# Kernel tuning notes

Measured on AMD Instinct MI355X. Metric: run time of the kernel, lower is better.

The kernel has to match this reference:

```python
import jax, jax.numpy as jnp
import numpy as np

B, H, W, C = 2, 256, 256, 180
WS, OWS, NH = 8, 12, 6  # window, overlap window, heads
RPB_N = (WS + OWS - 1) ** 2  # 361


def _ln(x, w, b):
    mu = x.mean(-1, keepdims=True)
    var = ((x - mu) ** 2).mean(-1, keepdims=True)
    return (x - mu) / jnp.sqrt(var + 1e-5) * w + b


def _dwt2(x):  # (b,h,w,c) -> (b,h/2,w/2,4c) haar, order [LL,LH,HL,HH]
    a = x[:, 0::2, 0::2]
    bb = x[:, 0::2, 1::2]
    cc = x[:, 1::2, 0::2]
    dd = x[:, 1::2, 1::2]
    ll = (a + bb + cc + dd) * 0.5
    lh = (-a - bb + cc + dd) * 0.5
    hl = (-a + bb - cc + dd) * 0.5
    hh = (a - bb - cc + dd) * 0.5
    return jnp.concatenate([ll, lh, hl, hh], axis=-1)


def _idwt2(y):  # (b,h2,w2,4c) -> (b,2h2,2w2,c)
    ll, lh, hl, hh = jnp.split(y, 4, axis=-1)
    a = (ll - lh - hl + hh) * 0.5
    bb = (ll - lh + hl - hh) * 0.5
    cc = (ll + lh - hl - hh) * 0.5
    dd = (ll + lh + hl + hh) * 0.5
    b_, h2, w2, c = a.shape
    even = jnp.stack([a, bb], axis=3).reshape(b_, h2, 2 * w2, c)
    odd = jnp.stack([cc, dd], axis=3).reshape(b_, h2, 2 * w2, c)
    return jnp.stack([even, odd], axis=2).reshape(b_, 2 * h2, 2 * w2, c)


def _win_part(x, ws):  # (b,h,w,c) -> (b*nw, ws, ws, c)
    b, h, w, c = x.shape
    x = x.reshape(b, h // ws, ws, w // ws, ws, c)
    return x.transpose(0, 1, 3, 2, 4, 5).reshape(-1, ws, ws, c)


def _win_rev(win, ws, h, w):  # inverse of _win_part
    b = win.shape[0] // ((h // ws) * (w // ws))
    x = win.reshape(b, h // ws, w // ws, ws, ws, -1)
    return x.transpose(0, 1, 3, 2, 4, 5).reshape(b, h, w, -1)


def _unfold_windows(x, ws, ows):  # nn.Unfold(kernel=ows, stride=ws, pad=ows-ws)
    b, hs, wss, c = x.shape
    pad = ows - ws
    xp = jnp.pad(x, ((0, 0), (pad, pad), (pad, pad), (0, 0)))
    nwh = hs // ws
    idx = (jnp.arange(nwh) * ws)[:, None] + jnp.arange(ows)[None, :]  # (nwh, ows)
    p = xp[:, idx][:, :, :, idx]  # (b, nwh, ows, nwh, ows, c)
    p = p.transpose(0, 1, 3, 2, 4, 5)  # (b, ih, iw, kh, kw, c)
    return p.reshape(b * nwh * nwh, ows * ows, c)


def _forward(x, cross_x, rpi, h, w, norm1_w, norm1_b, normc_w, normc_b,
             q_w, q_b, k_w, k_b, v_w, v_b, rpb, proj_w, proj_b,
             norm2_w, norm2_b, fc1_w, fc1_b, fc2_w, fc2_b):
    b, _, c = x.shape
    shortcut = x
    xn = _ln(x, norm1_w, norm1_b).reshape(b, h, w, c)
    _ = _ln(cross_x, normc_w, normc_b)  # computed in original wav branch, unused
    xd = _dwt2(xn)  # (b, h/2, w/2, 4c)
    q = xd @ q_w + q_b  # (b, h/2, w/2, c)
    k = xd @ k_w + k_b  # (b, h/2, w/2, c)
    v = xd @ v_w + v_b  # (b, h/2, w/2, 4c)
    scale = (c // NH) ** -0.5
    qw = _win_part(q, WS).reshape(-1, WS * WS, c)
    kw = _unfold_windows(k, WS, OWS)
    vw = _unfold_windows(v, WS, OWS)
    b_, nq = qw.shape[0], WS * WS
    n, d = OWS * OWS, c // NH
    qh = qw.reshape(b_, nq, NH, d).transpose(0, 2, 1, 3) * scale
    kh = kw.reshape(b_, n, NH, d).transpose(0, 2, 1, 3)
    vh = vw.reshape(b_, n, NH, 4 * d).transpose(0, 2, 1, 3)
    bias = rpb[rpi.reshape(-1)].reshape(nq, n, NH).transpose(2, 0, 1)  # (NH,nq,n)
    attn = jax.nn.softmax(jnp.einsum('bhqd,bhkd->bhqk', qh, kh) + bias[None], axis=-1)
    o = jnp.einsum('bhqk,bhkd->bhqd', attn, vh).transpose(0, 2, 1, 3).reshape(b_, nq, 4 * c)
    o = o.reshape(-1, WS, WS, 4 * c)
    xw = _win_rev(o, WS, h // 2, w // 2)  # (b, h/2, w/2, 4c)
    xr = _idwt2(xw).reshape(b, h * w, c)
    x1 = xr @ proj_w + proj_b + shortcut
    y = _ln(x1, norm2_w, norm2_b)
    y = jax.nn.gelu(y @ fc1_w + fc1_b, approximate=False) @ fc2_w + fc2_b
    return x1 + y


def setup_inputs() -> dict:
    key = jax.random.key(0)
    ks = jax.random.split(key, 12)
    nrm = lambda k, s: (jax.random.normal(k, s, jnp.float32) * 0.02)
    return {
        'x': jax.random.normal(ks[0], (B, H * W, C), jnp.float32),
        'cross_x': jax.random.normal(ks[1], (B, H * W, C), jnp.float32),
        'rpi': jax.random.randint(ks[2], (WS * WS, OWS * OWS), 0, RPB_N),
        'h': H, 'w': W,
        'norm1_w': jnp.ones((C,), jnp.float32), 'norm1_b': jnp.zeros((C,), jnp.float32),
        'normc_w': jnp.ones((C,), jnp.float32), 'normc_b': jnp.zeros((C,), jnp.float32),
        'q_w': nrm(ks[3], (4 * C, C)), 'q_b': jnp.zeros((C,), jnp.float32),
        'k_w': nrm(ks[4], (4 * C, C)), 'k_b': jnp.zeros((C,), jnp.float32),
        'v_w': nrm(ks[5], (4 * C, 4 * C)), 'v_b': jnp.zeros((4 * C,), jnp.float32),
        'rpb': nrm(ks[6], (RPB_N, NH)),
        'proj_w': nrm(ks[7], (C, C)), 'proj_b': jnp.zeros((C,), jnp.float32),
        'norm2_w': jnp.ones((C,), jnp.float32), 'norm2_b': jnp.zeros((C,), jnp.float32),
        'fc1_w': nrm(ks[8], (C, 2 * C)), 'fc1_b': jnp.zeros((2 * C,), jnp.float32),
        'fc2_w': nrm(ks[9], (2 * C, C)), 'fc2_b': jnp.zeros((C,), jnp.float32),
    }


def reference(x, cross_x, rpi, h, w, norm1_w, norm1_b, normc_w, normc_b,
              q_w, q_b, k_w, k_b, v_w, v_b, rpb, proj_w, proj_b,
              norm2_w, norm2_b, fc1_w, fc1_b, fc2_w, fc2_b):
    return _forward(x, cross_x, rpi, h, w, norm1_w, norm1_b, normc_w, normc_b,
                    q_w, q_b, k_w, k_b, v_w, v_b, rpb, proj_w, proj_b,
                    norm2_w, norm2_b, fc1_w, fc1_b, fc2_w, fc2_b)
```

## Files before the change

kernel.cpp:

```cpp
#include <hip/hip_runtime.h>
#include <hip/hip_bf16.h>
#include <stdint.h>

using bf16 = __hip_bfloat16;
typedef __attribute__((ext_vector_type(8))) short bf16x8;
typedef __attribute__((ext_vector_type(4))) float f32x4;

union U8 { uint4 u; bf16x8 h; };

static __device__ __forceinline__ float b2f(bf16 v) { return __bfloat162float(v); }
static __device__ __forceinline__ bf16  f2b(float v) { return __float2bfloat16(v); }
static __device__ __forceinline__ float toF(float v) { return v; }
static __device__ __forceinline__ float toF(bf16 v)  { return __bfloat162float(v); }
static __device__ __forceinline__ void stF(float* p, float v) { *p = v; }
static __device__ __forceinline__ void stF(bf16* p,  float v) { *p = f2b(v); }
static __device__ __forceinline__ float bfu(unsigned short x) {
  union { unsigned int i; float f; } z; z.i = ((unsigned int)x) << 16; return z.f;
}

__global__ __launch_bounds__(256) void convert_wt_kernel(
    const float* __restrict__ w, bf16* __restrict__ wt, int K, int N, int Kp)
{
  int idx = blockIdx.x * 256 + threadIdx.x;
  if (idx >= N * Kp) return;
  int n = idx / Kp, k = idx % Kp;
  float v = (k < K) ? w[(size_t)k * N + n] : 0.f;
  wt[idx] = f2b(v);
}

__global__ __launch_bounds__(256) void bias_pre_kernel(
    const int* __restrict__ rpi, const float* __restrict__ rpb, float* __restrict__ bias_f)
{
  int e = blockIdx.x * 256 + threadIdx.x;
  if (e >= 6 * 64 * 144) return;
  int hh = e / 9216, rk = e % 9216;
  bias_f[e] = rpb[rpi[rk] * 6 + hh];
}

__global__ __launch_bounds__(256) void ln_dwt_kernel(
    const float* __restrict__ x, const float* __restrict__ w, const float* __restrict__ bia,
    bf16* __restrict__ xd)
{
  __shared__ float nrm[4][180];
  int blk = blockIdx.x;
  int j = blk & 127; int i = (blk >> 7) & 127; int b = blk >> 14;
  int wave = threadIdx.x >> 6, lane = threadIdx.x & 63;
  int ty = wave >> 1, tx = wave & 1;
  size_t tok = (size_t)b * 65536 + (size_t)(2 * i + ty) * 256 + (size_t)(2 * j + tx);
  const float* xp = x + tok * 180;
  float v0 = xp[lane];
  float v1 = xp[lane + 64];
  float v2 = (lane < 52) ? xp[lane + 128] : 0.f;
  float s = v0 + v1 + v2, ss = v0 * v0 + v1 * v1 + v2 * v2;
  #pragma unroll
  for (int m = 32; m; m >>= 1) { s += __shfl_xor(s, m); ss += __shfl_xor(ss, m); }
  float mu = s * (1.f / 180.f);
  float rstd = rsqrtf(ss * (1.f / 180.f) - mu * mu + 1e-5f);
  nrm[wave][lane]      = (v0 - mu) * rstd * w[lane]      + bia[lane];
  nrm[wave][lane + 64] = (v1 - mu) * rstd * w[lane + 64] + bia[lane + 64];
  if (lane < 52)
    nrm[wave][lane + 128] = (v2 - mu) * rstd * w[lane + 128] + bia[lane + 128];
  __syncthreads();
  bf16* op = xd + (size_t)blk * 720;
  for (int o = threadIdx.x; o < 720; o += 256) {
    int g = o / 180, c = o % 180;
    float a = nrm[0][c], bb = nrm[1][c], cc = nrm[2][c], dd = nrm[3][c];
    float r = (g == 0) ? (a + bb + cc + dd)
            : (g == 1) ? (-a - bb + cc + dd)
            : (g == 2) ? (-a + bb - cc + dd)
                       : (a - bb - cc + dd);
    op[o] = f2b(r * 0.5f);
  }
}

__global__ __launch_bounds__(256) void ln_kernel(
    const bf16* __restrict__ x, const float* __restrict__ w, const float* __restrict__ bia,
    bf16* __restrict__ y)
{
  int wave = threadIdx.x >> 6, lane = threadIdx.x & 63;
  size_t tok = (size_t)blockIdx.x * 4 + wave;
  const bf16* xp = x + tok * 180;
  float v0 = b2f(xp[lane]);
  float v1 = b2f(xp[lane + 64]);
  float v2 = (lane < 52) ? b2f(xp[lane + 128]) : 0.f;
  float s = v0 + v1 + v2, ss = v0 * v0 + v1 * v1 + v2 * v2;
  #pragma unroll
  for (int m = 32; m; m >>= 1) { s += __shfl_xor(s, m); ss += __shfl_xor(ss, m); }
  float mu = s * (1.f / 180.f);
  float rstd = rsqrtf(ss * (1.f / 180.f) - mu * mu + 1e-5f);
  bf16* yp = y + tok * 192;
  yp[lane]      = f2b((v0 - mu) * rstd * w[lane]      + bia[lane]);
  yp[lane + 64] = f2b((v1 - mu) * rstd * w[lane + 64] + bia[lane + 64]);
  if (lane < 52)
    yp[lane + 128] = f2b((v2 - mu) * rstd * w[lane + 128] + bia[lane + 128]);
  else
    yp[lane + 128] = f2b(0.f);
}

template <int EP, typename TRes, typename TOut>
__global__ __launch_bounds__(256) void gemm_mfma(
    const bf16* __restrict__ A, const bf16* __restrict__ Wt,
    const float* __restrict__ bias, const TRes* __restrict__ res,
    TOut* __restrict__ out, int N, int KlimA, int lda, int Kp, int ldout, int ldres)
{
  __shared__ __align__(16) short Al[128 * 32];
  __shared__ __align__(16) short Bl[64 * 32];
  int tid = threadIdx.x;
  int wave = tid >> 6, lane = tid & 63;
  int wy = wave >> 1, wx = wave & 1;
  int m0 = blockIdx.x * 128, n0 = blockIdx.y * 64;

  f32x4 acc[4][2] = {};

  int ar = tid >> 2;
  int ac = (tid & 3) * 8;
  int brow = n0 + ar;
  int browc = (brow < N) ? brow : (N - 1);
  bool bvalid = (brow < N);
  const uint4* ga0 = (const uint4*)(A + (size_t)(m0 + ar) * lda + ac);
  const uint4* ga1 = (const uint4*)(A + (size_t)(m0 + 64 + ar) * lda + ac);
  const uint4* gb  = (const uint4*)(Wt + (size_t)browc * Kp + ac);

  int fm = lane & 15, quad = lane >> 4;
  const short* afp = &Al[(wy * 64 + fm) * 32 + quad * 8];
  const short* bfp = &Bl[(wx * 32 + fm) * 32 + quad * 8];

  for (int k0 = 0; k0 < Kp; k0 += 32) {
    bool avalid = (k0 + ac) < KlimA;
    uint4 za = avalid ? ga0[k0 / 8] : make_uint4(0, 0, 0, 0);
    uint4 zb = avalid ? ga1[k0 / 8] : make_uint4(0, 0, 0, 0);
    uint4 zc = bvalid ? gb[k0 / 8]  : make_uint4(0, 0, 0, 0);
    __syncthreads();
    *(uint4*)&Al[tid * 8]        = za;
    *(uint4*)&Al[2048 + tid * 8] = zb;
    *(uint4*)&Bl[tid * 8]        = zc;
    __syncthreads();

    bf16x8 af0 = *(const bf16x8*)(afp);
    bf16x8 af1 = *(const bf16x8*)(afp + 16 * 32);
    bf16x8 af2 = *(const bf16x8*)(afp + 32 * 32);
    bf16x8 af3 = *(const bf16x8*)(afp + 48 * 32);
    bf16x8 bf0 = *(const bf16x8*)(bfp);
    bf16x8 bf1 = *(const bf16x8*)(bfp + 16 * 32);

    acc[0][0] = __builtin_amdgcn_mfma_f32_16x16x32_bf16(af0, bf0, acc[0][0], 0, 0, 0);
    acc[0][1] = __builtin_amdgcn_mfma_f32_16x16x32_bf16(af0, bf1, acc[0][1], 0, 0, 0);
    acc[1][0] = __builtin_amdgcn_mfma_f32_16x16x32_bf16(af1, bf0, acc[1][0], 0, 0, 0);
    acc[1][1] = __builtin_amdgcn_mfma_f32_16x16x32_bf16(af1, bf1, acc[1][1], 0, 0, 0);
    acc[2][0] = __builtin_amdgcn_mfma_f32_16x16x32_bf16(af2, bf0, acc[2][0], 0, 0, 0);
    acc[2][1] = __builtin_amdgcn_mfma_f32_16x16x32_bf16(af2, bf1, acc[2][1], 0, 0, 0);
    acc[3][0] = __builtin_amdgcn_mfma_f32_16x16x32_bf16(af3, bf0, acc[3][0], 0, 0, 0);
    acc[3][1] = __builtin_amdgcn_mfma_f32_16x16x32_bf16(af3, bf1, acc[3][1], 0, 0, 0);
  }

  #pragma unroll
  for (int nt = 0; nt < 2; nt++) {
    int col = n0 + wx * 32 + nt * 16 + fm;
    if (col >= N) continue;
    float bv = bias[col];
    #pragma unroll
    for (int mt = 0; mt < 4; mt++) {
      int row0 = m0 + wy * 64 + mt * 16 + quad * 4;
      #pragma unroll
      for (int r = 0; r < 4; r++) {
        int row = row0 + r;
        float v = acc[mt][nt][r] + bv;
        if constexpr (EP == 1) v += toF(res[(size_t)row * ldres + col]);
        if constexpr (EP == 2) v = 0.5f * v * (1.f + erff(v * 0.70710678118654752f));
        stF(&out[(size_t)row * ldout + col], v);
      }
    }
  }
}

__global__ __launch_bounds__(256) void attn_kernel(
    const bf16* __restrict__ q, const bf16* __restrict__ k, const bf16* __restrict__ v,
    const float* __restrict__ bias_f, bf16* __restrict__ xw)
{
  __shared__ short tokl[160];
  __shared__ __align__(16) short Pl[64 * 168];
  __shared__ __align__(16) short Vt[128 * 168];
  const float scale = 0.18257418583505536f;
  int blk = blockIdx.x;
  int hh = blk % 6; int wid = blk / 6;
  int wj = wid & 15; int wi = (wid >> 4) & 15; int b = wid >> 8;
  int tid = threadIdx.x;
  int wave = tid >> 6, lane = tid & 63;
  int fm = lane & 15, quad = lane >> 4;
  const unsigned int* qu = (const unsigned int*)q;
  const unsigned int* ku = (const unsigned int*)k;
  const unsigned int* vu = (const unsigned int*)v;
  int hh15 = hh * 15, hh60 = hh * 60;

  if (tid < 144) {
    int ky = tid / 12, kx = tid % 12;
    int gy = wi * 8 - 4 + ky, gx = wj * 8 - 4 + kx;
    tokl[tid] = (gy >= 0 && gy < 128 && gx >= 0 && gx < 128)
              ? (short)(b * 16384 + gy * 128 + gx) : (short)-1;
  }
  __syncthreads();

  {
    int kg = tid & 15, oct = tid >> 4;
    int colx = (oct & 1) << 4;
    #pragma unroll
    for (int p = 0; p < 10; p++) {
      int kk = p * 16 + kg;
      int t = (kk < 144) ? (int)tokl[kk] : -1;
      U8 vv; vv.u = make_uint4(0, 0, 0, 0);
      if (oct < 15 && t >= 0)
        vv.u = *(const uint4*)(vu + (size_t)t * 360 + hh60 + oct * 4);
      short* wp = &Vt[oct * 8 * 168 + (kk ^ colx)];
      #pragma unroll
      for (int jj = 0; jj < 8; jj++) wp[jj * 168] = vv.h[jj];
    }
  }

  f32x4 sacc[9] = {};
  {
    U8 qf;
    int r = wave * 16 + fm;
    int gy = wi * 8 + (r >> 3), gx = wj * 8 + (r & 7);
    const unsigned int* qp = qu + (size_t)(b * 16384 + gy * 128 + gx) * 90 + hh15 + quad * 4;
    qf.u.x = qp[0]; qf.u.y = qp[1]; qf.u.z = qp[2]; qf.u.w = qp[3];
    if (quad == 3) qf.u.w = 0;
    #pragma unroll
    for (int nt = 0; nt < 9; nt++) {
      int t = (int)tokl[nt * 16 + fm];
      U8 kf; kf.u = make_uint4(0, 0, 0, 0);
      if (t >= 0) {
        const unsigned int* kp = ku + (size_t)t * 90 + hh15 + quad * 4;
        kf.u.x = kp[0]; kf.u.y = kp[1]; kf.u.z = kp[2]; kf.u.w = kp[3];
      }
      if (quad == 3) kf.u.w = 0;
      sacc[nt] = __builtin_amdgcn_mfma_f32_16x16x32_bf16(qf.h, kf.h, sacc[nt], 0, 0, 0);
    }
  }

  float sv[9][4];
  const float* bias_g = bias_f + hh * 9216;
  {
    #pragma unroll
    for (int r = 0; r < 4; r++) {
      int row = wave * 16 + quad * 4 + r;
      #pragma unroll
      for (int nt = 0; nt < 9; nt++)
        sv[nt][r] = sacc[nt][r] * scale + bias_g[row * 144 + nt * 16 + fm];
    }
    float mr[4], sr[4];
    #pragma unroll
    for (int r = 0; r < 4; r++) {
      float m = sv[0][r];
      #pragma unroll
      for (int nt = 1; nt < 9; nt++) m = fmaxf(m, sv[nt][r]);
      #pragma unroll
      for (int sh = 1; sh < 16; sh <<= 1) m = fmaxf(m, __shfl_xor(m, sh));
      mr[r] = m;
    }
    #pragma unroll
    for (int r = 0; r < 4; r++) {
      float s = 0.f;
      #pragma unroll
      for (int nt = 0; nt < 9; nt++) { sv[nt][r] = __expf(sv[nt][r] - mr[r]); s += sv[nt][r]; }
      #pragma unroll
      for (int sh = 1; sh < 16; sh <<= 1) s += __shfl_xor(s, sh);
      sr[r] = 1.f / s;
    }
    #pragma unroll
    for (int r = 0; r < 4; r++)
      #pragma unroll
      for (int nt = 0; nt < 9; nt++) sv[nt][r] *= sr[r];
  }

  #pragma unroll
  for (int r = 0; r < 4; r++) {
    int row = wave * 16 + quad * 4 + r;
    #pragma unroll
    for (int nt = 0; nt < 9; nt++)
      Pl[row * 168 + nt * 16 + fm] = (short)__bfloat16_as_ushort(f2b(sv[nt][r]));
  }
  #pragma unroll
  for (int j2 = 0; j2 < 2; j2++) {
    int idx = lane * 2 + j2;
    int row = wave * 16 + (idx >> 3);
    *(unsigned int*)&Pl[row * 168 + 144 + (idx & 7) * 2] = 0u;
  }
  __syncthreads();

  int sread = (fm & 8) << 1;
  bf16x8 pf[5];
  const short* prow = &Pl[(wave * 16 + fm) * 168];
  #pragma unroll
  for (int ks = 0; ks < 5; ks++) pf[ks] = *(const bf16x8*)&prow[ks * 32 + quad * 8];
  f32x4 oacc[8] = {};
  #pragma unroll
  for (int ks = 0; ks < 5; ks++) {
    #pragma unroll
    for (int nt = 0; nt < 8; nt++) {
      bf16x8 vf = *(const bf16x8*)&Vt[(nt * 16 + fm) * 168 + ((ks * 32 + quad * 8) ^ sread)];
      oacc[nt] = __builtin_amdgcn_mfma_f32_16x16x32_bf16(pf[ks], vf, oacc[nt], 0, 0, 0);
    }
  }
  #pragma unroll
  for (int nt = 0; nt < 8; nt++) {
    int col = nt * 16 + fm;
    if (col >= 120) continue;
    #pragma unroll
    for (int r = 0; r < 4; r++) {
      int row = wave * 16 + quad * 4 + r;
      int gy = wi * 8 + (row >> 3), gx = wj * 8 + (row & 7);
      xw[((size_t)b * 16384 + (size_t)gy * 128 + gx) * 720 + hh * 120 + col] = f2b(oacc[nt][r]);
    }
  }
}

__global__ __launch_bounds__(256) void idwt_kernel(
    const bf16* __restrict__ xw, bf16* __restrict__ xr)
{
  int gid = blockIdx.x * 256 + threadIdx.x;
  int cu = gid % 24;
  int tokn = gid / 24;
  int c = cu * 8;
  bf16* op = xr + (size_t)tokn * 192 + c;
  uint4 outv = make_uint4(0, 0, 0, 0);
  if (c < 184) {
    int x2 = tokn & 255, y2 = (tokn >> 8) & 255, bb = tokn >> 16;
    int ii = y2 >> 1, jj = x2 >> 1, py = y2 & 1, px = x2 & 1;
    const unsigned short* p = (const unsigned short*)xw
        + ((size_t)bb * 16384 + (size_t)ii * 128 + jj) * 720 + c;
    union QW { uint4 v; uint2 u[2]; unsigned short s[8]; } a_, b_, c_, d_, o_;
    a_.u[0] = *(const uint2*)(p);        a_.u[1] = *(const uint2*)(p + 4);
    b_.u[0] = *(const uint2*)(p + 180);  b_.u[1] = *(const uint2*)(p + 184);
    c_.u[0] = *(const uint2*)(p + 360);  c_.u[1] = *(const uint2*)(p + 364);
    d_.u[0] = *(const uint2*)(p + 540);  d_.u[1] = *(const uint2*)(p + 544);
    #pragma unroll
    for (int t = 0; t < 8; t++) {
      float ll = bfu(a_.s[t]), lh = bfu(b_.s[t]), hl = bfu(c_.s[t]), hv = bfu(d_.s[t]);
      float r;
      if (py == 0) r = (px == 0) ? (ll - lh - hl + hv) : (ll - lh + hl - hv);
      else         r = (px == 0) ? (ll + lh - hl - hv) : (ll + lh + hl + hv);
      o_.s[t] = (c + t < 180) ? __bfloat16_as_ushort(f2b(r * 0.5f)) : (unsigned short)0;
    }
    outv = o_.v;
  }
  *(uint4*)op = outv;
}

extern "C" void kernel_launch(void* const* d_in, const int* in_sizes, int n_in,
                              void* d_out, int out_size, void* d_ws, size_t ws_size,
                              hipStream_t stream) {
  (void)in_sizes; (void)n_in; (void)out_size; (void)ws_size;
  const float* x      = (const float*)d_in[0];
  const int*   rpi    = (const int*)  d_in[2];
  const float* n1w    = (const float*)d_in[5];
  const float* n1b    = (const float*)d_in[6];
  const float* q_w    = (const float*)d_in[9];
  const float* q_b    = (const float*)d_in[10];
  const float* k_w    = (const float*)d_in[11];
  const float* k_b    = (const float*)d_in[12];
  const float* v_w    = (const float*)d_in[13];
  const float* v_b    = (const float*)d_in[14];
  const float* rpb    = (const float*)d_in[15];
  const float* proj_w = (const float*)d_in[16];
  const float* proj_b = (const float*)d_in[17];
  const float* n2w    = (const float*)d_in[18];
  const float* n2b    = (const float*)d_in[19];
  const float* fc1_w  = (const float*)d_in[20];
  const float* fc1_b  = (const float*)d_in[21];
  const float* fc2_w  = (const float*)d_in[22];
  const float* fc2_b  = (const float*)d_in[23];
  float* out = (float*)d_out;

  bf16* xd  = (bf16*)d_ws;
  bf16* qb  = xd + 23592960;
  bf16* kb  = qb + 5898240;
  bf16* vb  = kb + 5898240;
  bf16* x1  = vb + 23592960;
  bf16* hb  = x1 + 23592960;
  bf16* wts = hb + 47185920;
  bf16* qwt  = wts;
  bf16* kwt  = qwt + 132480;
  bf16* vwt  = kwt + 132480;
  bf16* pwt  = vwt + 529920;
  bf16* f1wt = pwt + 34560;
  bf16* f2wt = f1wt + 69120;
  float* bias_f = (float*)(f2wt + 69120);
  bf16* xw = xd;
  bf16* xr = qb + 10223616;
  bf16* yb = xd;

  convert_wt_kernel<<<518,  256, 0, stream>>>(q_w,    qwt,  720, 180, 736);
  convert_wt_kernel<<<518,  256, 0, stream>>>(k_w,    kwt,  720, 180, 736);
  convert_wt_kernel<<<2071, 256, 0, stream>>>(v_w,    vwt,  720, 720, 736);
  convert_wt_kernel<<<135,  256, 0, stream>>>(proj_w, pwt,  180, 180, 192);
  convert_wt_kernel<<<270,  256, 0, stream>>>(fc1_w,  f1wt, 180, 360, 192);
  convert_wt_kernel<<<270,  256, 0, stream>>>(fc2_w,  f2wt, 360, 180, 384);
  bias_pre_kernel<<<216, 256, 0, stream>>>(rpi, rpb, bias_f);

  ln_dwt_kernel<<<32768, 256, 0, stream>>>(x, n1w, n1b, xd);
  gemm_mfma<0, float, bf16><<<dim3(256, 3),  256, 0, stream>>>(xd, qwt, q_b, nullptr, qb, 180, 720, 720, 736, 180, 0);
  gemm_mfma<0, float, bf16><<<dim3(256, 3),  256, 0, stream>>>(xd, kwt, k_b, nullptr, kb, 180, 720, 720, 736, 180, 0);
  gemm_mfma<0, float, bf16><<<dim3(256, 12), 256, 0, stream>>>(xd, vwt, v_b, nullptr, vb, 720, 720, 720, 736, 720, 0);
  attn_kernel<<<3072, 256, 0, stream>>>(qb, kb, vb, bias_f, xw);
  idwt_kernel<<<12288, 256, 0, stream>>>(xw, xr);
  gemm_mfma<1, float, bf16><<<dim3(1024, 3), 256, 0, stream>>>(xr, pwt, proj_b, x, x1, 180, 192, 192, 192, 180, 180);
  ln_kernel<<<32768, 256, 0, stream>>>(x1, n2w, n2b, yb);
  gemm_mfma<2, float, bf16><<<dim3(1024, 6), 256, 0, stream>>>(yb, f1wt, fc1_b, nullptr, hb, 360, 192, 192, 192, 360, 0);
  gemm_mfma<1, bf16, float><<<dim3(1024, 3), 256, 0, stream>>>(hb, f2wt, fc2_b, x1, out, 180, 360, 360, 384, 180, 180);
}
```

Before: 776.8 us.

## Fuse Q/K/V projections into one GEMM and widen GEMM N-tile to 192

Concatenates the Q, K and V weights and biases so a single GEMM writes one interleaved QKV buffer, and the attention kernel reads q, k and v from it at fixed offsets. The GEMM tile grows from 128x64 to 128x192 with register prefetch of the next K-slice, so the A tile is loaded far fewer times across N and global loads overlap with MFMA work. The trade-off is more accumulator registers per thread (24 f32x4), which may lower occupancy, and fewer blocks in the grid.

```diff
diff --git a/kernel.cpp b/kernel.cpp
--- a/kernel.cpp
+++ b/kernel.cpp
@@ -26,6 +26,15 @@
   int n = idx / Kp, k = idx % Kp;
   float v = (k < K) ? w[(size_t)k * N + n] : 0.f;
   wt[idx] = f2b(v);
+}
+
+__global__ __launch_bounds__(256) void concat_bias_kernel(
+    const float* __restrict__ qb, const float* __restrict__ kb,
+    const float* __restrict__ vb, float* __restrict__ o)
+{
+  int i = blockIdx.x * 256 + threadIdx.x;
+  if (i >= 1080) return;
+  o[i] = (i < 180) ? qb[i] : (i < 360) ? kb[i - 180] : vb[i - 360];
 }
 
 __global__ __launch_bounds__(256) void bias_pre_kernel(
@@ -104,58 +113,75 @@
     TOut* __restrict__ out, int N, int KlimA, int lda, int Kp, int ldout, int ldres)
 {
   __shared__ __align__(16) short Al[128 * 32];
-  __shared__ __align__(16) short Bl[64 * 32];
+  __shared__ __align__(16) short Bl[192 * 32];
   int tid = threadIdx.x;
   int wave = tid >> 6, lane = tid & 63;
   int wy = wave >> 1, wx = wave & 1;
-  int m0 = blockIdx.x * 128, n0 = blockIdx.y * 64;
-
-  f32x4 acc[4][2] = {};
-
-  int ar = tid >> 2;
-  int ac = (tid & 3) * 8;
-  int brow = n0 + ar;
-  int browc = (brow < N) ? brow : (N - 1);
-  bool bvalid = (brow < N);
-  const uint4* ga0 = (const uint4*)(A + (size_t)(m0 + ar) * lda + ac);
-  const uint4* ga1 = (const uint4*)(A + (size_t)(m0 + 64 + ar) * lda + ac);
-  const uint4* gb  = (const uint4*)(Wt + (size_t)browc * Kp + ac);
+  int m0 = blockIdx.x * 128, n0 = blockIdx.y * 192;
+
+  f32x4 acc[4][6] = {};
+
+  int ar0 = tid >> 2;
+  int ac  = (tid & 3) * 8;
+  const uint4* ga0 = (const uint4*)(A + (size_t)(m0 + ar0) * lda + ac);
+  const uint4* ga1 = (const uint4*)(A + (size_t)(m0 + 64 + ar0) * lda + ac);
+  int br0 = n0 + ar0, br1 = n0 + ar0 + 64, br2 = n0 + ar0 + 128;
+  bool bv0 = br0 < N, bv1 = br1 < N, bv2 = br2 < N;
+  const uint4* gb0 = (const uint4*)(Wt + (size_t)(bv0 ? br0 : 0) * Kp + ac);
+  const uint4* gb1 = (const uint4*)(Wt + (size_t)(bv1 ? br1 : 0) * Kp + ac);
+  const uint4* gb2 = (const uint4*)(Wt + (size_t)(bv2 ? br2 : 0) * Kp + ac);
 
   int fm = lane & 15, quad = lane >> 4;
   const short* afp = &Al[(wy * 64 + fm) * 32 + quad * 8];
-  const short* bfp = &Bl[(wx * 32 + fm) * 32 + quad * 8];
+  const short* bfp = &Bl[(wx * 96 + fm) * 32 + quad * 8];
+
+  const uint4 Z = make_uint4(0, 0, 0, 0);
+  uint4 za, zb, zc0, zc1, zc2;
+  {
+    bool av = ac < KlimA;
+    za  = av ? ga0[0] : Z;
+    zb  = av ? ga1[0] : Z;
+    zc0 = bv0 ? gb0[0] : Z;
+    zc1 = bv1 ? gb1[0] : Z;
+    zc2 = bv2 ? gb2[0] : Z;
+  }
 
   for (int k0 = 0; k0 < Kp; k0 += 32) {
-    bool avalid = (k0 + ac) < KlimA;
-    uint4 za = avalid ? ga0[k0 / 8] : make_uint4(0, 0, 0, 0);
-    uint4 zb = avalid ? ga1[k0 / 8] : make_uint4(0, 0, 0, 0);
-    uint4 zc = bvalid ? gb[k0 / 8]  : make_uint4(0, 0, 0, 0);
     __syncthreads();
     *(uint4*)&Al[tid * 8]        = za;
     *(uint4*)&Al[2048 + tid * 8] = zb;
-    *(uint4*)&Bl[tid * 8]        = zc;
+    *(uint4*)&Bl[tid * 8]        = zc0;
+    *(uint4*)&Bl[2048 + tid * 8] = zc1;
+    *(uint4*)&Bl[4096 + tid * 8] = zc2;
     __syncthreads();
+
+    int kn = k0 + 32;
+    if (kn < Kp) {
+      bool av = (kn + ac) < KlimA;
+      za  = av ? ga0[kn / 8] : Z;
+      zb  = av ? ga1[kn / 8] : Z;
+      zc0 = bv0 ? gb0[kn / 8] : Z;
+      zc1 = bv1 ? gb1[kn / 8] : Z;
+      zc2 = bv2 ? gb2[kn / 8] : Z;
+    }
 
     bf16x8 af0 = *(const bf16x8*)(afp);
     bf16x8 af1 = *(const bf16x8*)(afp + 16 * 32);
     bf16x8 af2 = *(const bf16x8*)(afp + 32 * 32);
     bf16x8 af3 = *(const bf16x8*)(afp + 48 * 32);
-    bf16x8 bf0 = *(const bf16x8*)(bfp);
-    bf16x8 bf1 = *(const bf16x8*)(bfp + 16 * 32);
-
-    acc[0][0] = __builtin_amdgcn_mfma_f32_16x16x32_bf16(af0, bf0, acc[0][0], 0, 0, 0);
-    acc[0][1] = __builtin_amdgcn_mfma_f32_16x16x32_bf16(af0, bf1, acc[0][1], 0, 0, 0);
-    acc[1][0] = __builtin_amdgcn_mfma_f32_16x16x32_bf16(af1, bf0, acc[1][0], 0, 0, 0);
-    acc[1][1] = __builtin_amdgcn_mfma_f32_16x16x32_bf16(af1, bf1, acc[1][1], 0, 0, 0);
-    acc[2][0] = __builtin_amdgcn_mfma_f32_16x16x32_bf16(af2, bf0, acc[2][0], 0, 0, 0);
-    acc[2][1] = __builtin_amdgcn_mfma_f32_16x16x32_bf16(af2, bf1, acc[2][1], 0, 0, 0);
-    acc[3][0] = __builtin_amdgcn_mfma_f32_16x16x32_bf16(af3, bf0, acc[3][0], 0, 0, 0);
-    acc[3][1] = __builtin_amdgcn_mfma_f32_16x16x32_bf16(af3, bf1, acc[3][1], 0, 0, 0);
-  }
-
-  #pragma unroll
-  for (int nt = 0; nt < 2; nt++) {
-    int col = n0 + wx * 32 + nt * 16 + fm;
+    #pragma unroll
+    for (int nt = 0; nt < 6; nt++) {
+      bf16x8 bfr = *(const bf16x8*)(bfp + nt * 16 * 32);
+      acc[0][nt] = __builtin_amdgcn_mfma_f32_16x16x32_bf16(af0, bfr, acc[0][nt], 0, 0, 0);
+      acc[1][nt] = __builtin_amdgcn_mfma_f32_16x16x32_bf16(af1, bfr, acc[1][nt], 0, 0, 0);
+      acc[2][nt] = __builtin_amdgcn_mfma_f32_16x16x32_bf16(af2, bfr, acc[2][nt], 0, 0, 0);
+      acc[3][nt] = __builtin_amdgcn_mfma_f32_16x16x32_bf16(af3, bfr, acc[3][nt], 0, 0, 0);
+    }
+  }
+
+  #pragma unroll
+  for (int nt = 0; nt < 6; nt++) {
+    int col = n0 + wx * 96 + nt * 16 + fm;
     if (col >= N) continue;
     float bv = bias[col];
     #pragma unroll
@@ -174,8 +200,7 @@
 }
 
 __global__ __launch_bounds__(256) void attn_kernel(
-    const bf16* __restrict__ q, const bf16* __restrict__ k, const bf16* __restrict__ v,
-    const float* __restrict__ bias_f, bf16* __restrict__ xw)
+    const bf16* __restrict__ qkv, const float* __restrict__ bias_f, bf16* __restrict__ xw)
 {
   __shared__ short tokl[160];
   __shared__ __align__(16) short Pl[64 * 168];
@@ -187,9 +212,7 @@
   int tid = threadIdx.x;
   int wave = tid >> 6, lane = tid & 63;
   int fm = lane & 15, quad = lane >> 4;
-  const unsigned int* qu = (const unsigned int*)q;
-  const unsigned int* ku = (const unsigned int*)k;
-  const unsigned int* vu = (const unsigned int*)v;
+  const unsigned int* qkvu = (const unsigned int*)qkv;
   int hh15 = hh * 15, hh60 = hh * 60;
 
   if (tid < 144) {
@@ -209,7 +232,7 @@
       int t = (kk < 144) ? (int)tokl[kk] : -1;
       U8 vv; vv.u = make_uint4(0, 0, 0, 0);
       if (oct < 15 && t >= 0)
-        vv.u = *(const uint4*)(vu + (size_t)t * 360 + hh60 + oct * 4);
+        vv.u = *(const uint4*)(qkvu + (size_t)t * 540 + 180 + hh60 + oct * 4);
       short* wp = &Vt[oct * 8 * 168 + (kk ^ colx)];
       #pragma unroll
       for (int jj = 0; jj < 8; jj++) wp[jj * 168] = vv.h[jj];
@@ -221,7 +244,7 @@
     U8 qf;
     int r = wave * 16 + fm;
     int gy = wi * 8 + (r >> 3), gx = wj * 8 + (r & 7);
-    const unsigned int* qp = qu + (size_t)(b * 16384 + gy * 128 + gx) * 90 + hh15 + quad * 4;
+    const unsigned int* qp = qkvu + (size_t)(b * 16384 + gy * 128 + gx) * 540 + hh15 + quad * 4;
     qf.u.x = qp[0]; qf.u.y = qp[1]; qf.u.z = qp[2]; qf.u.w = qp[3];
     if (quad == 3) qf.u.w = 0;
     #pragma unroll
@@ -229,7 +252,7 @@
       int t = (int)tokl[nt * 16 + fm];
       U8 kf; kf.u = make_uint4(0, 0, 0, 0);
       if (t >= 0) {
-        const unsigned int* kp = ku + (size_t)t * 90 + hh15 + quad * 4;
+        const unsigned int* kp = qkvu + (size_t)t * 540 + 90 + hh15 + quad * 4;
         kf.u.x = kp[0]; kf.u.y = kp[1]; kf.u.z = kp[2]; kf.u.w = kp[3];
       }
       if (quad == 3) kf.u.w = 0;
@@ -372,39 +395,35 @@
   float* out = (float*)d_out;
 
   bf16* xd  = (bf16*)d_ws;
-  bf16* qb  = xd + 23592960;
-  bf16* kb  = qb + 5898240;
-  bf16* vb  = kb + 5898240;
-  bf16* x1  = vb + 23592960;
+  bf16* qkv = xd + 23592960;
+  bf16* x1  = qkv + 35389440;
   bf16* hb  = x1 + 23592960;
   bf16* wts = hb + 47185920;
-  bf16* qwt  = wts;
-  bf16* kwt  = qwt + 132480;
-  bf16* vwt  = kwt + 132480;
-  bf16* pwt  = vwt + 529920;
+  bf16* qkvwt = wts;
+  bf16* pwt  = qkvwt + 794880;
   bf16* f1wt = pwt + 34560;
   bf16* f2wt = f1wt + 69120;
   float* bias_f = (float*)(f2wt + 69120);
+  float* qkv_b  = bias_f + 55296;
   bf16* xw = xd;
-  bf16* xr = qb + 10223616;
+  bf16* xr = qkv + 10223616;
   bf16* yb = xd;
 
-  convert_wt_kernel<<<518,  256, 0, stream>>>(q_w,    qwt,  720, 180, 736);
-  convert_wt_kernel<<<518,  256, 0, stream>>>(k_w,    kwt,  720, 180, 736);
-  convert_wt_kernel<<<2071, 256, 0, stream>>>(v_w,    vwt,  720, 720, 736);
+  convert_wt_kernel<<<518,  256, 0, stream>>>(q_w,    qkvwt,          720, 180, 736);
+  convert_wt_kernel<<<518,  256, 0, stream>>>(k_w,    qkvwt + 132480, 720, 180, 736);
+  convert_wt_kernel<<<2071, 256, 0, stream>>>(v_w,    qkvwt + 264960, 720, 720, 736);
   convert_wt_kernel<<<135,  256, 0, stream>>>(proj_w, pwt,  180, 180, 192);
   convert_wt_kernel<<<270,  256, 0, stream>>>(fc1_w,  f1wt, 180, 360, 192);
   convert_wt_kernel<<<270,  256, 0, stream>>>(fc2_w,  f2wt, 360, 180, 384);
+  concat_bias_kernel<<<5, 256, 0, stream>>>(q_b, k_b, v_b, qkv_b);
   bias_pre_kernel<<<216, 256, 0, stream>>>(rpi, rpb, bias_f);
 
   ln_dwt_kernel<<<32768, 256, 0, stream>>>(x, n1w, n1b, xd);
-  gemm_mfma<0, float, bf16><<<dim3(256, 3),  256, 0, stream>>>(xd, qwt, q_b, nullptr, qb, 180, 720, 720, 736, 180, 0);
-  gemm_mfma<0, float, bf16><<<dim3(256, 3),  256, 0, stream>>>(xd, kwt, k_b, nullptr, kb, 180, 720, 720, 736, 180, 0);
-  gemm_mfma<0, float, bf16><<<dim3(256, 12), 256, 0, stream>>>(xd, vwt, v_b, nullptr, vb, 720, 720, 720, 736, 720, 0);
-  attn_kernel<<<3072, 256, 0, stream>>>(qb, kb, vb, bias_f, xw);
+  gemm_mfma<0, float, bf16><<<dim3(256, 6),  256, 0, stream>>>(xd, qkvwt, qkv_b, nullptr, qkv, 1080, 720, 720, 736, 1080, 0);
+  attn_kernel<<<3072, 256, 0, stream>>>(qkv, bias_f, xw);
   idwt_kernel<<<12288, 256, 0, stream>>>(xw, xr);
-  gemm_mfma<1, float, bf16><<<dim3(1024, 3), 256, 0, stream>>>(xr, pwt, proj_b, x, x1, 180, 192, 192, 192, 180, 180);
+  gemm_mfma<1, float, bf16><<<dim3(1024, 1), 256, 0, stream>>>(xr, pwt, proj_b, x, x1, 180, 192, 192, 192, 180, 180);
   ln_kernel<<<32768, 256, 0, stream>>>(x1, n2w, n2b, yb);
-  gemm_mfma<2, float, bf16><<<dim3(1024, 6), 256, 0, stream>>>(yb, f1wt, fc1_b, nullptr, hb, 360, 192, 192, 192, 360, 0);
-  gemm_mfma<1, bf16, float><<<dim3(1024, 3), 256, 0, stream>>>(hb, f2wt, fc2_b, x1, out, 180, 360, 360, 384, 180, 180);
-}
+  gemm_mfma<2, float, bf16><<<dim3(1024, 2), 256, 0, stream>>>(yb, f1wt, fc1_b, nullptr, hb, 360, 192, 192, 192, 360, 0);
+  gemm_mfma<1, bf16, float><<<dim3(1024, 1), 256, 0, stream>>>(hb, f2wt, fc2_b, x1, out, 180, 360, 360, 384, 180, 180);
+}
```

Result: faster. 729.5 us (-6.1%).
